# Optimization experiments

Measured on AMD Instinct MI355X. Metric: run time of the kernel, lower is better.

The kernel has to match this reference:

```python
import jax, jax.numpy as jnp
import numpy as np

N, E = 50000, 800000
IN_C, HID, OUT_C, HEADS = 768, 64, 8, 8
NEG_SLOPE = 0.2
BN_EPS = 1e-5


def _bn(x, g, b, m, v):
    # BatchNorm1d in eval mode with running stats
    return (x - m) * jax.lax.rsqrt(v + BN_EPS) * g + b


def _gat_conv(x, W, att_src, att_dst, bias, src, dst, n):
    H, C = att_src.shape
    xw = (x @ W).reshape(n, H, C)                      # [N,H,C]
    a_src = jnp.sum(xw * att_src, axis=-1)             # [N,H]
    a_dst = jnp.sum(xw * att_dst, axis=-1)             # [N,H]
    alpha = jax.nn.leaky_relu(a_src[src] + a_dst[dst], NEG_SLOPE)  # [E',H]
    amax = jax.ops.segment_max(alpha, dst, num_segments=n)          # [N,H]
    ex = jnp.exp(alpha - amax[dst])
    denom = jax.ops.segment_sum(ex, dst, num_segments=n)            # [N,H]
    coef = ex / denom[dst]                                          # [E',H]
    out = jax.ops.segment_sum(xw[src] * coef[:, :, None], dst, num_segments=n)
    return out.reshape(n, H * C) + bias


def setup_inputs() -> dict:
    key = jax.random.key(0)
    ks = jax.random.split(key, 24)
    d = {}
    d['x'] = jax.random.normal(ks[0], (N, IN_C), dtype=jnp.float32)
    d['edge_index'] = jax.random.randint(ks[1], (2, E), 0, N, dtype=jnp.int32)
    d['proj_W'] = jax.random.normal(ks[2], (IN_C, HID), dtype=jnp.float32) * (IN_C ** -0.5)
    d['proj_b'] = jnp.zeros((HID,), jnp.float32)
    for i, kb in zip((1, 2, 3), (ks[3], ks[4], ks[5])):
        k1, k2 = jax.random.split(kb)
        d[f'bn{i}_g'] = jnp.ones((HID,), jnp.float32)
        d[f'bn{i}_b'] = jnp.zeros((HID,), jnp.float32)
        d[f'bn{i}_m'] = jax.random.normal(k1, (HID,), dtype=jnp.float32) * 0.1
        d[f'bn{i}_v'] = jax.random.uniform(k2, (HID,), dtype=jnp.float32, minval=0.5, maxval=1.5)
    C1 = HID // HEADS
    d['W1'] = jax.random.normal(ks[6], (HID, HEADS * C1), dtype=jnp.float32) * (HID ** -0.5)
    d['att_src1'] = jax.random.normal(ks[7], (HEADS, C1), dtype=jnp.float32) * 0.1
    d['att_dst1'] = jax.random.normal(ks[8], (HEADS, C1), dtype=jnp.float32) * 0.1
    d['b1'] = jnp.zeros((HEADS * C1,), jnp.float32)
    d['W2'] = jax.random.normal(ks[9], (HID, HID), dtype=jnp.float32) * (HID ** -0.5)
    d['att_src2'] = jax.random.normal(ks[10], (1, HID), dtype=jnp.float32) * 0.1
    d['att_dst2'] = jax.random.normal(ks[11], (1, HID), dtype=jnp.float32) * 0.1
    d['b2'] = jnp.zeros((HID,), jnp.float32)
    d['cls_W'] = jax.random.normal(ks[12], (HID, OUT_C), dtype=jnp.float32) * (HID ** -0.5)
    d['cls_b'] = jnp.zeros((OUT_C,), jnp.float32)
    return d


def reference(x, edge_index, proj_W, proj_b,
              bn1_g, bn1_b, bn1_m, bn1_v,
              W1, att_src1, att_dst1, b1,
              bn2_g, bn2_b, bn2_m, bn2_v,
              W2, att_src2, att_dst2, b2,
              bn3_g, bn3_b, bn3_m, bn3_v,
              cls_W, cls_b):
    n = x.shape[0]
    # add self-loops (PyG GATConv default)
    loop = jnp.arange(n, dtype=edge_index.dtype)
    src = jnp.concatenate([edge_index[0], loop])
    dst = jnp.concatenate([edge_index[1], loop])

    h = x @ proj_W + proj_b
    h = jax.nn.elu(_bn(h, bn1_g, bn1_b, bn1_m, bn1_v))
    identity = h
    h = _gat_conv(h, W1, att_src1, att_dst1, b1, src, dst, n)
    h = jax.nn.elu(_bn(h, bn2_g, bn2_b, bn2_m, bn2_v) + identity)
    identity = h
    h = _gat_conv(h, W2, att_src2, att_dst2, b2, src, dst, n)
    h = jax.nn.elu(_bn(h, bn3_g, bn3_b, bn3_m, bn3_v) + identity)
    return h @ cls_W + cls_b
```

## Files before the change

kernel.cpp:

```cpp
#include <hip/hip_runtime.h>

typedef __bf16 bf16;
typedef __attribute__((ext_vector_type(8))) __bf16 bf16x8;
typedef __attribute__((ext_vector_type(4))) float f32x4;
typedef unsigned short u16;

#define LSTR  40
#define LSTR2 72
#define BN_EPS 1e-5f

__global__ __launch_bounds__(256) void k_prep(
        const float* __restrict__ W0, const float* __restrict__ W1, const float* __restrict__ W2,
        bf16* __restrict__ Wt0, bf16* __restrict__ Wt1, bf16* __restrict__ Wt2,
        int* __restrict__ cnt, int n)
{
    int i = blockIdx.x*256 + threadIdx.x;
    const int T = 768*64 + 8192;
    if (i < 768*64)            { int k = i>>6, n_ = i&63;                  Wt0[n_*768+k] = (bf16)W0[i]; }
    else if (i < 768*64+4096)  { int j = i-768*64;      int k=j>>6,c=j&63; Wt1[c*64+k]  = (bf16)W1[j]; }
    else if (i < T)            { int j = i-768*64-4096; int k=j>>6,c=j&63; Wt2[c*64+k]  = (bf16)W2[j]; }
    int j = i - T;
    if (j >= 0 && j < n) cnt[j] = 0;
}

__global__ __launch_bounds__(256) void k_fused_proj(
        const float* __restrict__ A, const bf16* __restrict__ Bt,
        const bf16* __restrict__ W1t, int M,
        const float* __restrict__ pb, const float* __restrict__ g,
        const float* __restrict__ bb, const float* __restrict__ mm, const float* __restrict__ vv,
        const float* __restrict__ att_s, const float* __restrict__ att_d,
        bf16* __restrict__ h0b, bf16* __restrict__ xwb,
        float* __restrict__ a_s, float* __restrict__ a_d)
{
    const int K = 768;
    __shared__ bf16 xs[2][64*LSTR];
    __shared__ bf16 bs[2][64*LSTR];
    __shared__ bf16 hs [64*LSTR2];
    __shared__ bf16 w1s[64*LSTR2];
    __shared__ float sC[64], cC[64];

    int t = threadIdx.x;
    int w = t >> 6, lane = t & 63;
    int q = lane >> 4, l16 = lane & 15;
    int row0 = blockIdx.x * 64;
    int sRow = t >> 2, sK = (t & 3) * 8;

    if (t < 64) {
        float s = rsqrtf(vv[t] + BN_EPS) * g[t];
        sC[t] = s;
        cC[t] = (pb[t] - mm[t]) * s + bb[t];
    }
    {
        int r = t >> 2, c0 = (t & 3) * 16;
        *(bf16x8*)(w1s + r*LSTR2 + c0)     = *(const bf16x8*)(W1t + r*64 + c0);
        *(bf16x8*)(w1s + r*LSTR2 + c0 + 8) = *(const bf16x8*)(W1t + r*64 + c0 + 8);
    }

    auto loadA = [&](int k0) -> bf16x8 {
        bf16x8 xv;
        #pragma unroll
        for (int i = 0; i < 8; ++i) xv[i] = (bf16)0.f;
        int gr = row0 + sRow;
        if (gr < M) {
            const float* ap = A + (size_t)gr*K + k0 + sK;
            float4 f0 = *(const float4*)ap;
            float4 f1 = *(const float4*)(ap + 4);
            xv[0]=(bf16)f0.x; xv[1]=(bf16)f0.y; xv[2]=(bf16)f0.z; xv[3]=(bf16)f0.w;
            xv[4]=(bf16)f1.x; xv[5]=(bf16)f1.y; xv[6]=(bf16)f1.z; xv[7]=(bf16)f1.w;
        }
        return xv;
    };
    auto loadB = [&](int k0) -> bf16x8 {
        return *(const bf16x8*)(Bt + (size_t)sRow*K + k0 + sK);
    };

    f32x4 acc[4];
    #pragma unroll
    for (int i = 0; i < 4; ++i) { acc[i][0]=0.f; acc[i][1]=0.f; acc[i][2]=0.f; acc[i][3]=0.f; }

    bf16x8 xv = loadA(0);
    bf16x8 bv = loadB(0);
    *(bf16x8*)(&xs[0][sRow*LSTR + sK]) = xv;
    *(bf16x8*)(&bs[0][sRow*LSTR + sK]) = bv;
    __syncthreads();

    int cur = 0;
    for (int k0 = 0; k0 < K; k0 += 32) {
        if (k0 + 32 < K) {
            xv = loadA(k0 + 32);
            bv = loadB(k0 + 32);
        }
        bf16x8 af = *(bf16x8*)(&xs[cur][(w*16 + l16)*LSTR + q*8]);
        #pragma unroll
        for (int tt = 0; tt < 4; ++tt) {
            bf16x8 bfr = *(bf16x8*)(&bs[cur][(tt*16 + l16)*LSTR + q*8]);
            acc[tt] = __builtin_amdgcn_mfma_f32_16x16x32_bf16(af, bfr, acc[tt], 0, 0, 0);
        }
        if (k0 + 32 < K) {
            *(bf16x8*)(&xs[cur^1][sRow*LSTR + sK]) = xv;
            *(bf16x8*)(&bs[cur^1][sRow*LSTR + sK]) = bv;
            __syncthreads();
            cur ^= 1;
        }
    }

    #pragma unroll
    for (int tt = 0; tt < 4; ++tt) {
        int col = tt*16 + l16;
        #pragma unroll
        for (int r = 0; r < 4; ++r) {
            int rl = w*16 + q*4 + r;
            float val = acc[tt][r] * sC[col] + cC[col];
            val = val > 0.f ? val : __expf(val) - 1.f;
            hs[rl*LSTR2 + col] = (bf16)val;
            int row = row0 + rl;
            if (row < M) h0b[(size_t)row*64 + col] = (bf16)val;
        }
    }
    __syncthreads();

    f32x4 acc2[4];
    #pragma unroll
    for (int i = 0; i < 4; ++i) { acc2[i][0]=0.f; acc2[i][1]=0.f; acc2[i][2]=0.f; acc2[i][3]=0.f; }
    #pragma unroll
    for (int ks = 0; ks < 2; ++ks) {
        bf16x8 af = *(bf16x8*)(&hs[(w*16 + l16)*LSTR2 + ks*32 + q*8]);
        #pragma unroll
        for (int tt = 0; tt < 4; ++tt) {
            bf16x8 bfr = *(bf16x8*)(&w1s[(tt*16 + l16)*LSTR2 + ks*32 + q*8]);
            acc2[tt] = __builtin_amdgcn_mfma_f32_16x16x32_bf16(af, bfr, acc2[tt], 0, 0, 0);
        }
    }

    #pragma unroll
    for (int tt = 0; tt < 4; ++tt) {
        int col = tt*16 + l16;
        #pragma unroll
        for (int r = 0; r < 4; ++r) {
            int row = row0 + w*16 + q*4 + r;
            if (row < M) xwb[(size_t)row*64 + col] = (bf16)acc2[tt][r];
        }
    }
    #pragma unroll
    for (int r = 0; r < 4; ++r) {
        int row = row0 + w*16 + q*4 + r;
        float ps[4], pd[4];
        #pragma unroll
        for (int tt = 0; tt < 4; ++tt) {
            int col = tt*16 + l16;
            ps[tt] = acc2[tt][r] * att_s[col];
            pd[tt] = acc2[tt][r] * att_d[col];
        }
        #pragma unroll
        for (int off = 1; off < 8; off <<= 1) {
            #pragma unroll
            for (int tt = 0; tt < 4; ++tt) {
                ps[tt] += __shfl_xor(ps[tt], off);
                pd[tt] += __shfl_xor(pd[tt], off);
            }
        }
        if ((l16 & 7) == 0 && row < M) {
            int hb = l16 >> 3;
            #pragma unroll
            for (int tt = 0; tt < 4; ++tt) {
                a_s[row*8 + 2*tt + hb] = ps[tt];
                a_d[row*8 + 2*tt + hb] = pd[tt];
            }
        }
    }
}

template<int MODE, bool ABF, int H>
__global__ __launch_bounds__(256) void k_gemm64(
        const void* __restrict__ Av, const bf16* __restrict__ Bt, int M, int K,
        const float* __restrict__ pb, const float* __restrict__ g, const float* __restrict__ bb,
        const float* __restrict__ mm, const float* __restrict__ vv,
        bf16* __restrict__ outB,
        float* __restrict__ a_s, float* __restrict__ a_d,
        const float* __restrict__ att_s, const float* __restrict__ att_d)
{
    __shared__ bf16 xs[64*LSTR];
    __shared__ bf16 bs[64*LSTR];
    __shared__ float sC[64], cC[64];

    int t = threadIdx.x;
    int w = t >> 6, lane = t & 63;
    int q = lane >> 4, l16 = lane & 15;
    int row0 = blockIdx.x * 64;
    int sRow = t >> 2, sK = (t & 3) * 8;

    auto loadA = [&](int k0) -> bf16x8 {
        bf16x8 xv;
        #pragma unroll
        for (int i = 0; i < 8; ++i) xv[i] = (bf16)0.f;
        int gr = row0 + sRow;
        if (gr < M) {
            if constexpr (ABF) {
                xv = *(const bf16x8*)((const bf16*)Av + (size_t)gr*K + k0 + sK);
            } else {
                const float* ap = (const float*)Av + (size_t)gr*K + k0 + sK;
                float4 f0 = *(const float4*)ap;
                float4 f1 = *(const float4*)(ap + 4);
                xv[0]=(bf16)f0.x; xv[1]=(bf16)f0.y; xv[2]=(bf16)f0.z; xv[3]=(bf16)f0.w;
                xv[4]=(bf16)f1.x; xv[5]=(bf16)f1.y; xv[6]=(bf16)f1.z; xv[7]=(bf16)f1.w;
            }
        }
        return xv;
    };
    auto loadB = [&](int k0) -> bf16x8 {
        return *(const bf16x8*)(Bt + (size_t)sRow*K + k0 + sK);
    };

    f32x4 acc[4];
    #pragma unroll
    for (int i = 0; i < 4; ++i) { acc[i][0]=0.f; acc[i][1]=0.f; acc[i][2]=0.f; acc[i][3]=0.f; }

    bf16x8 xv = loadA(0);
    bf16x8 bv = loadB(0);

    for (int k0 = 0; k0 < K; k0 += 32) {
        *(bf16x8*)(xs + sRow*LSTR + sK) = xv;
        *(bf16x8*)(bs + sRow*LSTR + sK) = bv;
        __syncthreads();
        if (k0 + 32 < K) {
            xv = loadA(k0 + 32);
            bv = loadB(k0 + 32);
        }
        bf16x8 af = *(bf16x8*)(xs + (w*16 + l16)*LSTR + q*8);
        #pragma unroll
        for (int tt = 0; tt < 4; ++tt) {
            bf16x8 bfr = *(bf16x8*)(bs + (tt*16 + l16)*LSTR + q*8);
            acc[tt] = __builtin_amdgcn_mfma_f32_16x16x32_bf16(af, bfr, acc[tt], 0, 0, 0);
        }
        __syncthreads();
    }

    if constexpr (MODE == 0) {
        if (t < 64) {
            float s = rsqrtf(vv[t] + BN_EPS) * g[t];
            sC[t] = s;
            cC[t] = (pb[t] - mm[t]) * s + bb[t];
        }
        __syncthreads();
    }

    #pragma unroll
    for (int tt = 0; tt < 4; ++tt) {
        int col = tt*16 + l16;
        #pragma unroll
        for (int r = 0; r < 4; ++r) {
            int row = row0 + w*16 + q*4 + r;
            if (row < M) {
                float val = acc[tt][r];
                if constexpr (MODE == 0) {
                    val = val * sC[col] + cC[col];
                    val = val > 0.f ? val : __expf(val) - 1.f;
                }
                outB[(size_t)row*64 + col] = (bf16)val;
            }
        }
    }

    if constexpr (MODE == 1) {
        #pragma unroll
        for (int r = 0; r < 4; ++r) {
            int row = row0 + w*16 + q*4 + r;
            if constexpr (H == 1) {
                float ps = 0.f, pd = 0.f;
                #pragma unroll
                for (int tt = 0; tt < 4; ++tt) {
                    int col = tt*16 + l16;
                    ps += acc[tt][r] * att_s[col];
                    pd += acc[tt][r] * att_d[col];
                }
                #pragma unroll
                for (int off = 1; off < 16; off <<= 1) {
                    ps += __shfl_xor(ps, off);
                    pd += __shfl_xor(pd, off);
                }
                if (l16 == 0 && row < M) { a_s[row] = ps; a_d[row] = pd; }
            } else {
                float ps[4], pd[4];
                #pragma unroll
                for (int tt = 0; tt < 4; ++tt) {
                    int col = tt*16 + l16;
                    ps[tt] = acc[tt][r] * att_s[col];
                    pd[tt] = acc[tt][r] * att_d[col];
                }
                #pragma unroll
                for (int off = 1; off < 8; off <<= 1) {
                    #pragma unroll
                    for (int tt = 0; tt < 4; ++tt) {
                        ps[tt] += __shfl_xor(ps[tt], off);
                        pd[tt] += __shfl_xor(pd[tt], off);
                    }
                }
                if ((l16 & 7) == 0 && row < M) {
                    int hb = l16 >> 3;
                    #pragma unroll
                    for (int tt = 0; tt < 4; ++tt) {
                        a_s[row*8 + 2*tt + hb] = ps[tt];
                        a_d[row*8 + 2*tt + hb] = pd[tt];
                    }
                }
            }
        }
    }
}

__global__ __launch_bounds__(256) void k_count(const int* __restrict__ dst, int E, int* cnt) {
    int i = blockIdx.x*256 + threadIdx.x;
    if (i < E) atomicAdd(&cnt[dst[i]], 1);
}
__global__ __launch_bounds__(256) void k_scan_block(const int* __restrict__ cnt,
        int* __restrict__ rp, int* __restrict__ bsum, int n) {
    __shared__ int s[256];
    int t = threadIdx.x, v = blockIdx.x*256 + t;
    int x = (v < n) ? cnt[v] : 0;
    s[t] = x; __syncthreads();
    for (int off = 1; off < 256; off <<= 1) {
        int y = (t >= off) ? s[t-off] : 0;
        __syncthreads();
        s[t] += y;
        __syncthreads();
    }
    if (v < n) rp[v+1] = s[t];
    if (t == 255) bsum[blockIdx.x] = s[255];
}
__global__ __launch_bounds__(256) void k_finalize(int* __restrict__ rp, const int* __restrict__ bsum,
        const int* __restrict__ cnt, int* __restrict__ cursor, int n, int nb) {
    __shared__ int s[256];
    int t = threadIdx.x;
    int x = (t < nb) ? bsum[t] : 0;
    s[t] = x; __syncthreads();
    for (int off = 1; off < 256; off <<= 1) {
        int y = (t >= off) ? s[t-off] : 0;
        __syncthreads();
        s[t] += y;
        __syncthreads();
    }
    int v = blockIdx.x*256 + t;
    if (v < n) {
        int b = v >> 8;
        int off0 = (b == 0) ? 0 : s[b-1];
        int val = rp[v+1] + off0;
        rp[v+1] = val;
        cursor[v] = val - cnt[v];
        if (v == 0) rp[0] = 0;
    }
}
__global__ __launch_bounds__(256) void k_scatter(const int* __restrict__ src, const int* __restrict__ dst,
        int E, int* __restrict__ cursor, u16* __restrict__ in_src) {
    int i = blockIdx.x*256 + threadIdx.x;
    if (i < E) {
        int pos = atomicAdd(&cursor[dst[i]], 1);
        in_src[pos] = (u16)src[i];
    }
}

template<int H, bool CLS>
__global__ __launch_bounds__(256) void k_gat_agg(const bf16* __restrict__ xwb,
        const float* __restrict__ a_src, const float* __restrict__ a_dst,
        const int* __restrict__ rp, const u16* __restrict__ in_src,
        const float* __restrict__ bias,
        const float* __restrict__ g, const float* __restrict__ bb,
        const float* __restrict__ mm, const float* __restrict__ vv,
        const bf16* __restrict__ resid, bf16* __restrict__ outB, float* __restrict__ outF,
        const float* __restrict__ clsW, const float* __restrict__ clsb, int n)
{
    int wv = (blockIdx.x*256 + threadIdx.x) >> 6;
    int lane = threadIdx.x & 63;
    if (wv >= n) return;
    int h = (H == 8) ? (lane >> 3) : 0;
    float adst = a_dst[wv*H + h];

    float aself = a_src[wv*H + h] + adst;
    aself = (aself > 0.f) ? aself : 0.2f*aself;
    float eself = __expf(aself);
    float acc = eself * (float)xwb[(size_t)wv*64 + lane];
    float den = eself;

    int beg = rp[wv], end = rp[wv+1];
    int e = beg;
    for (; e + 8 <= end; e += 8) {
        int u[8];
        #pragma unroll
        for (int i = 0; i < 8; ++i) u[i] = (int)in_src[e+i];
        float s[8], xr[8];
        #pragma unroll
        for (int i = 0; i < 8; ++i) s[i] = a_src[u[i]*H + h];
        #pragma unroll
        for (int i = 0; i < 8; ++i) xr[i] = (float)xwb[(size_t)u[i]*64 + lane];
        #pragma unroll
        for (int i = 0; i < 8; ++i) {
            float a = s[i] + adst;
            a = (a > 0.f) ? a : 0.2f*a;
            float ex = __expf(a);
            acc += ex * xr[i];
            den += ex;
        }
    }
    for (; e < end; ++e) {
        int u = (int)in_src[e];
        float al = a_src[u*H + h] + adst;
        al = (al > 0.f) ? al : 0.2f*al;
        float ex = __expf(al);
        acc += ex * (float)xwb[(size_t)u*64 + lane];
        den += ex;
    }
    float val = acc/den + bias[lane];
    float sc = rsqrtf(vv[lane] + BN_EPS) * g[lane];
    val = (val - mm[lane]) * sc + bb[lane];
    val += (float)resid[(size_t)wv*64 + lane];
    val = (val > 0.f) ? val : __expf(val) - 1.f;

    if constexpr (!CLS) {
        outB[(size_t)wv*64 + lane] = (bf16)val;
    } else {
        float keep = 0.f;
        #pragma unroll
        for (int o = 0; o < 8; ++o) {
            float p = val * clsW[lane*8 + o];
            #pragma unroll
            for (int off = 1; off < 64; off <<= 1) p += __shfl_xor(p, off);
            if (lane == o) keep = p + clsb[o];
        }
        if (lane < 8) outF[(size_t)wv*8 + lane] = keep;
    }
}

extern "C" void kernel_launch(void* const* d_in, const int* in_sizes, int n_in,
                              void* d_out, int out_size, void* d_ws, size_t ws_size,
                              hipStream_t stream)
{
    const float* x      = (const float*)d_in[0];
    const int*   ei     = (const int*)  d_in[1];
    const float* proj_W = (const float*)d_in[2];
    const float* proj_b = (const float*)d_in[3];
    const float* bn1_g  = (const float*)d_in[4];
    const float* bn1_b  = (const float*)d_in[5];
    const float* bn1_m  = (const float*)d_in[6];
    const float* bn1_v  = (const float*)d_in[7];
    const float* bn2_g  = (const float*)d_in[8];
    const float* bn2_b  = (const float*)d_in[9];
    const float* bn2_m  = (const float*)d_in[10];
    const float* bn2_v  = (const float*)d_in[11];
    const float* bn3_g  = (const float*)d_in[12];
    const float* bn3_b  = (const float*)d_in[13];
    const float* bn3_m  = (const float*)d_in[14];
    const float* bn3_v  = (const float*)d_in[15];
    const float* W1     = (const float*)d_in[16];
    const float* att_s1 = (const float*)d_in[17];
    const float* att_d1 = (const float*)d_in[18];
    const float* b1     = (const float*)d_in[19];
    const float* W2     = (const float*)d_in[20];
    const float* att_s2 = (const float*)d_in[21];
    const float* att_d2 = (const float*)d_in[22];
    const float* b2     = (const float*)d_in[23];
    const float* cls_W  = (const float*)d_in[24];
    const float* cls_b  = (const float*)d_in[25];

    const int N = in_sizes[0] / 768;
    const int E = in_sizes[1] / 2;
    const int* srce = ei;
    const int* dste = ei + E;

    char* p = (char*)d_ws;
    auto carve = [&](size_t bytes) -> void* {
        void* r = (void*)p;
        p += (bytes + 255) & ~(size_t)255;
        return r;
    };
    bf16*  Wt0    = (bf16*) carve((size_t)64*768*2);
    bf16*  Wt1    = (bf16*) carve((size_t)64*64*2);
    bf16*  Wt2    = (bf16*) carve((size_t)64*64*2);
    bf16*  h0b    = (bf16*) carve((size_t)N*64*2);
    bf16*  h1b    = (bf16*) carve((size_t)N*64*2);
    bf16*  xwb    = (bf16*) carve((size_t)N*64*2);
    float* a_s    = (float*)carve((size_t)N*8*4);
    float* a_d    = (float*)carve((size_t)N*8*4);
    int*   cnt    = (int*)  carve((size_t)N*4);
    int*   rp     = (int*)  carve((size_t)(N+1)*4);
    int*   cursor = (int*)  carve((size_t)N*4);
    int*   bsum   = (int*)  carve(1024);
    u16*   in_src = (u16*)  carve((size_t)E*2);

    const int nb = (N + 255) / 256;
    const int PREP = 768*64 + 8192;

    k_prep<<<(PREP + N + 255)/256, 256, 0, stream>>>(proj_W, W1, W2, Wt0, Wt1, Wt2, cnt, N);

    k_count<<<(E + 255)/256, 256, 0, stream>>>(dste, E, cnt);
    k_scan_block<<<nb, 256, 0, stream>>>(cnt, rp, bsum, N);
    k_finalize<<<nb, 256, 0, stream>>>(rp, bsum, cnt, cursor, N, nb);
    k_scatter<<<(E + 255)/256, 256, 0, stream>>>(srce, dste, E, cursor, in_src);

    k_fused_proj<<<(N + 63)/64, 256, 0, stream>>>(x, Wt0, Wt1, N,
            proj_b, bn1_g, bn1_b, bn1_m, bn1_v, att_s1, att_d1,
            h0b, xwb, a_s, a_d);

    k_gat_agg<8, false><<<(N + 3)/4, 256, 0, stream>>>(xwb, a_s, a_d, rp, in_src,
            b1, bn2_g, bn2_b, bn2_m, bn2_v, h0b, h1b, nullptr, nullptr, nullptr, N);

    k_gemm64<1, true, 1><<<(N + 63)/64, 256, 0, stream>>>(h1b, Wt2, N, 64,
            nullptr, nullptr, nullptr, nullptr, nullptr, xwb, a_s, a_d, att_s2, att_d2);
    k_gat_agg<1, true><<<(N + 3)/4, 256, 0, stream>>>(xwb, a_s, a_d, rp, in_src,
            b2, bn3_g, bn3_b, bn3_m, bn3_v, h1b, nullptr, (float*)d_out, cls_W, cls_b, N);
}
```

Before: 489.4 us.

## Split GAT aggregation wave into four edge groups with 4-channel vector loads

The per-node aggregation wave now splits its 64 lanes into 4 edge groups of 16 lanes. Each lane handles 4 channels through 8-byte bf16 loads, so four edges are processed in parallel instead of one edge across 64 lanes. Partial sums are combined with cross-group shuffles, and the classifier reduction is restructured to batch its shuffles. This aims to raise memory-level parallelism and cut per-edge instruction count on the latency-bound gather, at the cost of extra shuffle reductions and a masked tail loop.

```diff
diff --git a/kernel.cpp b/kernel.cpp
--- a/kernel.cpp
+++ b/kernel.cpp
@@ -2,12 +2,16 @@
 
 typedef __bf16 bf16;
 typedef __attribute__((ext_vector_type(8))) __bf16 bf16x8;
+typedef __attribute__((ext_vector_type(4))) __bf16 bf16x4;
 typedef __attribute__((ext_vector_type(4))) float f32x4;
 typedef unsigned short u16;
 
 #define LSTR  40
 #define LSTR2 72
 #define BN_EPS 1e-5f
+
+__device__ inline float bfl(unsigned int w) { return __uint_as_float(w << 16); }
+__device__ inline float bfh(unsigned int w) { return __uint_as_float(w & 0xffff0000u); }
 
 __global__ __launch_bounds__(256) void k_prep(
         const float* __restrict__ W0, const float* __restrict__ W1, const float* __restrict__ W2,
@@ -363,7 +367,7 @@
         const float* __restrict__ a_src, const float* __restrict__ a_dst,
         const int* __restrict__ rp, const u16* __restrict__ in_src,
         const float* __restrict__ bias,
-        const float* __restrict__ g, const float* __restrict__ bb,
+        const float* __restrict__ g_, const float* __restrict__ bb,
         const float* __restrict__ mm, const float* __restrict__ vv,
         const bf16* __restrict__ resid, bf16* __restrict__ outB, float* __restrict__ outF,
         const float* __restrict__ clsW, const float* __restrict__ clsb, int n)
@@ -371,61 +375,102 @@
     int wv = (blockIdx.x*256 + threadIdx.x) >> 6;
     int lane = threadIdx.x & 63;
     if (wv >= n) return;
-    int h = (H == 8) ? (lane >> 3) : 0;
-    float adst = a_dst[wv*H + h];
-
-    float aself = a_src[wv*H + h] + adst;
-    aself = (aself > 0.f) ? aself : 0.2f*aself;
-    float eself = __expf(aself);
-    float acc = eself * (float)xwb[(size_t)wv*64 + lane];
-    float den = eself;
+    int eg = lane >> 4;
+    int s  = lane & 15;
+    int c0 = s * 4;
+    int h  = (H == 8) ? (s >> 1) : 0;
+    float adst = a_dst[(size_t)wv*H + h];
+
+    float a0 = 0.f, a1 = 0.f, a2 = 0.f, a3 = 0.f, den = 0.f;
+
+    if (eg == 0) {
+        float asf = a_src[(size_t)wv*H + h] + adst;
+        asf = (asf > 0.f) ? asf : 0.2f*asf;
+        float ex = __expf(asf);
+        uint2 xw = *(const uint2*)(xwb + (size_t)wv*64 + c0);
+        a0 = ex*bfl(xw.x); a1 = ex*bfh(xw.x); a2 = ex*bfl(xw.y); a3 = ex*bfh(xw.y);
+        den = ex;
+    }
 
     int beg = rp[wv], end = rp[wv+1];
     int e = beg;
     for (; e + 8 <= end; e += 8) {
-        int u[8];
-        #pragma unroll
-        for (int i = 0; i < 8; ++i) u[i] = (int)in_src[e+i];
-        float s[8], xr[8];
-        #pragma unroll
-        for (int i = 0; i < 8; ++i) s[i] = a_src[u[i]*H + h];
-        #pragma unroll
-        for (int i = 0; i < 8; ++i) xr[i] = (float)xwb[(size_t)u[i]*64 + lane];
-        #pragma unroll
-        for (int i = 0; i < 8; ++i) {
-            float a = s[i] + adst;
-            a = (a > 0.f) ? a : 0.2f*a;
-            float ex = __expf(a);
-            acc += ex * xr[i];
-            den += ex;
-        }
-    }
-    for (; e < end; ++e) {
-        int u = (int)in_src[e];
-        float al = a_src[u*H + h] + adst;
-        al = (al > 0.f) ? al : 0.2f*al;
-        float ex = __expf(al);
-        acc += ex * (float)xwb[(size_t)u*64 + lane];
+        int u0 = (int)in_src[e + eg];
+        int u1 = (int)in_src[e + 4 + eg];
+        float s0 = a_src[(size_t)u0*H + h];
+        float s1 = a_src[(size_t)u1*H + h];
+        uint2 x0 = *(const uint2*)(xwb + (size_t)u0*64 + c0);
+        uint2 x1 = *(const uint2*)(xwb + (size_t)u1*64 + c0);
+        float al0 = s0 + adst; al0 = (al0 > 0.f) ? al0 : 0.2f*al0;
+        float al1 = s1 + adst; al1 = (al1 > 0.f) ? al1 : 0.2f*al1;
+        float e0 = __expf(al0), e1 = __expf(al1);
+        a0 += e0*bfl(x0.x) + e1*bfl(x1.x);
+        a1 += e0*bfh(x0.x) + e1*bfh(x1.x);
+        a2 += e0*bfl(x0.y) + e1*bfl(x1.y);
+        a3 += e0*bfh(x0.y) + e1*bfh(x1.y);
+        den += e0 + e1;
+    }
+    for (; e < end; e += 4) {
+        int idx = e + eg;
+        bool act = idx < end;
+        int u = act ? (int)in_src[idx] : 0;
+        float sv = a_src[(size_t)u*H + h];
+        uint2 xw = *(const uint2*)(xwb + (size_t)u*64 + c0);
+        float al = sv + adst; al = (al > 0.f) ? al : 0.2f*al;
+        float ex = act ? __expf(al) : 0.f;
+        a0 += ex*bfl(xw.x); a1 += ex*bfh(xw.x); a2 += ex*bfl(xw.y); a3 += ex*bfh(xw.y);
         den += ex;
     }
-    float val = acc/den + bias[lane];
-    float sc = rsqrtf(vv[lane] + BN_EPS) * g[lane];
-    val = (val - mm[lane]) * sc + bb[lane];
-    val += (float)resid[(size_t)wv*64 + lane];
-    val = (val > 0.f) ? val : __expf(val) - 1.f;
+
+    #pragma unroll
+    for (int off = 16; off < 64; off <<= 1) {
+        a0 += __shfl_xor(a0, off);
+        a1 += __shfl_xor(a1, off);
+        a2 += __shfl_xor(a2, off);
+        a3 += __shfl_xor(a3, off);
+        den += __shfl_xor(den, off);
+    }
+
+    float inv = 1.f / den;
+    uint2 rz = *(const uint2*)(resid + (size_t)wv*64 + c0);
+    float v[4]  = { a0*inv, a1*inv, a2*inv, a3*inv };
+    float rv[4] = { bfl(rz.x), bfh(rz.x), bfl(rz.y), bfh(rz.y) };
+    #pragma unroll
+    for (int j = 0; j < 4; ++j) {
+        int c = c0 + j;
+        float val = v[j] + bias[c];
+        float sc = rsqrtf(vv[c] + BN_EPS) * g_[c];
+        val = (val - mm[c]) * sc + bb[c];
+        val += rv[j];
+        val = (val > 0.f) ? val : __expf(val) - 1.f;
+        v[j] = val;
+    }
 
     if constexpr (!CLS) {
-        outB[(size_t)wv*64 + lane] = (bf16)val;
+        if (eg == 0) {
+            bf16x4 o;
+            o[0] = (bf16)v[0]; o[1] = (bf16)v[1]; o[2] = (bf16)v[2]; o[3] = (bf16)v[3];
+            *(bf16x4*)(outB + (size_t)wv*64 + c0) = o;
+        }
     } else {
-        float keep = 0.f;
+        if (eg != 0) { v[0] = 0.f; v[1] = 0.f; v[2] = 0.f; v[3] = 0.f; }
+        float p[8];
         #pragma unroll
         for (int o = 0; o < 8; ++o) {
-            float p = val * clsW[lane*8 + o];
+            p[o] = v[0]*clsW[(c0+0)*8+o] + v[1]*clsW[(c0+1)*8+o]
+                 + v[2]*clsW[(c0+2)*8+o] + v[3]*clsW[(c0+3)*8+o];
+        }
+        #pragma unroll
+        for (int off = 1; off < 64; off <<= 1) {
             #pragma unroll
-            for (int off = 1; off < 64; off <<= 1) p += __shfl_xor(p, off);
-            if (lane == o) keep = p + clsb[o];
-        }
-        if (lane < 8) outF[(size_t)wv*8 + lane] = keep;
+            for (int o = 0; o < 8; ++o) p[o] += __shfl_xor(p[o], off);
+        }
+        if (lane < 8) {
+            float r = 0.f;
+            #pragma unroll
+            for (int o = 0; o < 8; ++o) if (lane == o) r = p[o] + clsb[o];
+            outF[(size_t)wv*8 + lane] = r;
+        }
     }
 }
 
```

New measurement: 482.8 us. Within noise of the previous version (-1.4%).
